# Optimization experiments

Hardware: AMD Instinct MI355X
Metric: run time of the kernel (lower is better)

## Reference

```python
import jax, jax.numpy as jnp
import numpy as np

SEQ_LEN = 4096
D_IN = 1024
D_OUT = 1024


def setup_inputs() -> dict:
    key = jax.random.key(0)
    k_x, k_q, k_k, k_v = jax.random.split(key, 4)
    s = 1.0 / np.sqrt(D_IN)
    return {
        "x": jax.random.normal(k_x, (SEQ_LEN, D_IN), dtype=jnp.float32),
        "W_query": jax.random.normal(k_q, (D_IN, D_OUT), dtype=jnp.float32) * s,
        "W_key": jax.random.normal(k_k, (D_IN, D_OUT), dtype=jnp.float32) * s,
        "W_value": jax.random.normal(k_v, (D_IN, D_OUT), dtype=jnp.float32) * s,
    }


def reference(x, W_query, W_key, W_value):
    # QKV projections (Linear without bias): [S, d_out]
    q = x @ W_query
    k = x @ W_key
    v = x @ W_value
    # Full S x S score matrix, causal mask, scaled softmax
    scores = q @ k.T  # [S, S]
    seq_len = x.shape[0]
    causal = jnp.tril(jnp.ones((seq_len, seq_len), dtype=bool))
    scores = jnp.where(causal, scores, -jnp.inf)
    scale = 1.0 / jnp.sqrt(jnp.asarray(k.shape[-1], dtype=scores.dtype))
    attn = jax.nn.softmax(scores * scale, axis=-1)
    return attn @ v  # [S, d_out]
```

## Files before the change

### kernel.cpp

```cpp
#include <hip/hip_runtime.h>
#include <math.h>

#define SEQ 4096
#define DIM 1024

typedef unsigned short u16;
typedef __attribute__((ext_vector_type(8))) short short8;
typedef __attribute__((ext_vector_type(4))) float floatx4;
typedef __attribute__((ext_vector_type(4))) unsigned short us4;

__device__ __forceinline__ float bf2f(u16 u) {
    union { unsigned int i; float f; } c; c.i = ((unsigned int)u) << 16; return c.f;
}
__device__ __forceinline__ u16 f2bf(float f) {
    union { float f; unsigned int i; } c; c.f = f;
    return (u16)((c.i + 0x7fffu + ((c.i >> 16) & 1u)) >> 16);
}
__device__ __forceinline__ void gload_lds16(const u16* g, u16* l) {
    __builtin_amdgcn_global_load_lds((const __attribute__((address_space(1))) void*)g,
                                     (__attribute__((address_space(3))) void*)l, 16, 0, 0);
}

__device__ __forceinline__ void pipe256(const u16* __restrict__ A,
                                        const u16* __restrict__ B,
                                        u16 (&As)[2][8192], u16 (&Bs)[2][4096],
                                        int lda, int ldb, int row0, int col0,
                                        int wave, int lane,
                                        floatx4 (&acc)[4][4]) {
    const int wm = wave & 3, wn = wave >> 2;
    const int sa0 = wave * 128 + lane, sa1 = sa0 + 64;
    const int ra0 = sa0 >> 2, qa0 = ((sa0 & 3) ^ ((sa0 >> 3) & 3)) * 8;
    const int ra1 = sa1 >> 2, qa1 = ((sa1 & 3) ^ ((sa1 >> 3) & 3)) * 8;
    const int sb0 = wave * 64 + lane;
    const int rb0 = sb0 >> 2, qb0 = ((sb0 & 3) ^ ((sb0 >> 3) & 3)) * 8;
    const u16* aP0 = A + (size_t)(row0 + ra0) * lda + qa0;
    const u16* aP1 = A + (size_t)(row0 + ra1) * lda + qa1;
    const u16* bP0 = B + (size_t)(col0 + rb0) * ldb + qb0;
    const int lA = wave * 1024;
    const int lB = wave * 512;
    const int frow = lane & 15;
    const int xq = (((lane >> 4) ^ ((frow >> 1) & 3))) * 8;

    auto stage = [&](int c) {
        gload_lds16(aP0, &As[c][lA]);
        gload_lds16(aP1, &As[c][lA + 512]);
        gload_lds16(bP0, &Bs[c][lB]);
        aP0 += 32; aP1 += 32; bP0 += 32;
    };

    stage(0);
    __syncthreads();
    for (int it = 0; it < 32; ++it) {
        const int cur = it & 1;
        if (it < 31) stage(cur ^ 1);
        short8 af[4], bfr[4];
#pragma unroll
        for (int t = 0; t < 4; ++t) {
            af[t]  = *(const short8*)&As[cur][(wm * 64 + t * 16 + frow) * 32 + xq];
            bfr[t] = *(const short8*)&Bs[cur][(wn * 64 + t * 16 + frow) * 32 + xq];
        }
#pragma unroll
        for (int mt = 0; mt < 4; ++mt)
#pragma unroll
            for (int nt = 0; nt < 4; ++nt)
                acc[mt][nt] = __builtin_amdgcn_mfma_f32_16x16x32_bf16(
                    af[mt], bfr[nt], acc[mt][nt], 0, 0, 0);
        __syncthreads();
    }
}

__global__ __launch_bounds__(512) void proj256(const u16* __restrict__ xb,
                                               const u16* __restrict__ Wt,
                                               u16* __restrict__ QK,
                                               u16* __restrict__ Vt,
                                               float scale0) {
    __shared__ u16 As[2][8192], Bs[2][4096];
    const int row0 = blockIdx.y * 256;
    const int col0 = blockIdx.x * 128;
    const int tid = threadIdx.x, wave = tid >> 6, lane = tid & 63;
    const int wm = wave & 3, wn = wave >> 2;

    floatx4 acc[4][4] = {};
    pipe256(xb, Wt, As, Bs, DIM, DIM, row0, col0, wave, lane, acc);

    const int cr = (lane >> 4) * 4, cc = lane & 15;
    if (col0 >= 2048) {
#pragma unroll
        for (int mt = 0; mt < 4; ++mt)
#pragma unroll
            for (int nt = 0; nt < 4; ++nt) {
                const int row = row0 + wm * 64 + mt * 16 + cr;
                const int col = (col0 - 2048) + wn * 64 + nt * 16 + cc;
                us4 o = { f2bf(acc[mt][nt][0]), f2bf(acc[mt][nt][1]),
                          f2bf(acc[mt][nt][2]), f2bf(acc[mt][nt][3]) };
                *(us4*)&Vt[(size_t)col * SEQ + row] = o;
            }
    } else {
        const float sc = (col0 < 1024) ? scale0 : 1.0f;
#pragma unroll
        for (int mt = 0; mt < 4; ++mt)
#pragma unroll
            for (int nt = 0; nt < 4; ++nt)
#pragma unroll
                for (int r = 0; r < 4; ++r) {
                    const int row = row0 + wm * 64 + mt * 16 + cr + r;
                    const int col = col0 + wn * 64 + nt * 16 + cc;
                    QK[(size_t)row * 2048 + col] = f2bf(acc[mt][nt][r] * sc);
                }
    }
}

__global__ __launch_bounds__(512) void scores256(const u16* __restrict__ QK,
                                                 u16* __restrict__ E,
                                                 float* __restrict__ Lsum) {
    __shared__ u16 As[2][8192], Bs[2][4096];
    const int t = blockIdx.x;
    int R = (int)((sqrtf(4.0f * t + 1.0f) - 1.0f) * 0.5f);
    while ((R + 1) * (R + 2) + R + 1 - 1 < t + 1) ++R;
    while (R * R + R > t) --R;
    const int bx = t - (R * R + R);
    const int row0 = R * 256, col0 = bx * 128;
    const int tid = threadIdx.x, wave = tid >> 6, lane = tid & 63;
    const int wm = wave & 3, wn = wave >> 2;

    floatx4 acc[4][4] = {};
    pipe256(QK, QK + 1024, As, Bs, 2048, 2048, row0, col0, wave, lane, acc);

    const int cr = (lane >> 4) * 4, cc = lane & 15;
#pragma unroll
    for (int mt = 0; mt < 4; ++mt) {
#pragma unroll
        for (int r = 0; r < 4; ++r) {
            const int grow = row0 + wm * 64 + mt * 16 + cr + r;
            float rowsum = 0.f;
#pragma unroll
            for (int nt = 0; nt < 4; ++nt) {
                const int gcol = col0 + wn * 64 + nt * 16 + cc;
                const float e = (gcol <= grow) ? __expf(acc[mt][nt][r]) : 0.f;
                rowsum += e;
                E[(size_t)grow * SEQ + gcol] = f2bf(e);
            }
            rowsum += __shfl_xor(rowsum, 1);
            rowsum += __shfl_xor(rowsum, 2);
            rowsum += __shfl_xor(rowsum, 4);
            rowsum += __shfl_xor(rowsum, 8);
            if (cc == 0) atomicAdd(&Lsum[grow], rowsum);
        }
    }
}

__global__ __launch_bounds__(256) void pv64(const u16* __restrict__ E,
                                            const u16* __restrict__ Vt,
                                            float* __restrict__ O,
                                            const float* __restrict__ Lsum) {
    const int lin = blockIdx.x + (blockIdx.y << 4);
    const int c = lin & 7;
    const int j = lin >> 3;
    const int x = j & 15;
    const int m = j >> 4;
    const unsigned long long PK = 0x2F3F20301F0F1000ULL;
    const int base = (int)((PK >> (m * 8)) & 0x3F);
    const int r = base + ((m & 2) ? -c : c);
    const int row0 = r * 64;
    const int col0 = x * 64;
    const int kend = row0 + 64;

    __shared__ u16 As[3][2048], Bs[3][2048];

    const int tid  = threadIdx.x;
    const int wave = tid >> 6;
    const int lane = tid & 63;
    const int wm = wave & 1;
    const int wn = wave >> 1;

    const int s0 = wave * 64 + lane;
    const int r0 = s0 >> 2, q0 = ((s0 & 3) ^ ((s0 >> 3) & 3)) * 8;
    const u16* aP = E  + (size_t)(row0 + r0) * SEQ + q0;
    const u16* bP = Vt + (size_t)(col0 + r0) * SEQ + q0;
    const int l0 = wave * 512;

    floatx4 acc[2][2] = {};
    const int niter = kend >> 5;
    const int frow = lane & 15;
    const int xq = (((lane >> 4) ^ ((frow >> 1) & 3))) * 8;
    const int mrow0 = wm * 32, nrow0 = wn * 32;

    auto stage = [&](int cb) {
        gload_lds16(aP, &As[cb][l0]);
        gload_lds16(bP, &Bs[cb][l0]);
        aP += 32; bP += 32;
    };
    stage(0);
    stage(1);

    auto compute_tile = [&](int cb) {
        short8 af[2], bfr[2];
#pragma unroll
        for (int t = 0; t < 2; ++t) {
            af[t]  = *(const short8*)&As[cb][(mrow0 + t * 16 + frow) * 32 + xq];
            bfr[t] = *(const short8*)&Bs[cb][(nrow0 + t * 16 + frow) * 32 + xq];
        }
#pragma unroll
        for (int mt = 0; mt < 2; ++mt)
#pragma unroll
            for (int nt = 0; nt < 2; ++nt)
                acc[mt][nt] = __builtin_amdgcn_mfma_f32_16x16x32_bf16(
                    af[mt], bfr[nt], acc[mt][nt], 0, 0, 0);
    };

    int cur = 0, pre = 2;
    for (int it = 0; it < niter - 2; ++it) {
        asm volatile("s_waitcnt vmcnt(2)\n\ts_barrier" ::: "memory");
        short8 af[2], bfr[2];
#pragma unroll
        for (int t = 0; t < 2; ++t) {
            af[t]  = *(const short8*)&As[cur][(mrow0 + t * 16 + frow) * 32 + xq];
            bfr[t] = *(const short8*)&Bs[cur][(nrow0 + t * 16 + frow) * 32 + xq];
        }
        stage(pre);
#pragma unroll
        for (int mt = 0; mt < 2; ++mt)
#pragma unroll
            for (int nt = 0; nt < 2; ++nt)
                acc[mt][nt] = __builtin_amdgcn_mfma_f32_16x16x32_bf16(
                    af[mt], bfr[nt], acc[mt][nt], 0, 0, 0);
        cur = (cur == 2) ? 0 : cur + 1;
        pre = (pre == 2) ? 0 : pre + 1;
    }
    asm volatile("s_waitcnt vmcnt(2)\n\ts_barrier" ::: "memory");
    compute_tile(cur);
    cur = (cur == 2) ? 0 : cur + 1;
    asm volatile("s_waitcnt vmcnt(0)\n\ts_barrier" ::: "memory");
    compute_tile(cur);

    const int cr = (lane >> 4) * 4, cc = lane & 15;
#pragma unroll
    for (int mt = 0; mt < 2; ++mt)
#pragma unroll
        for (int rr = 0; rr < 4; ++rr) {
            const int grow = row0 + wm * 32 + mt * 16 + cr + rr;
            const float invl = __builtin_amdgcn_rcpf(Lsum[grow]);
#pragma unroll
            for (int nt = 0; nt < 2; ++nt) {
                const int col = col0 + wn * 32 + nt * 16 + cc;
                O[(size_t)grow * DIM + col] = acc[mt][nt][rr] * invl;
            }
        }
}

__global__ __launch_bounds__(256) void prep(const float* __restrict__ x,
                                            const float* __restrict__ W0,
                                            const float* __restrict__ W1,
                                            const float* __restrict__ W2,
                                            u16* __restrict__ xb,
                                            u16* __restrict__ Wt,
                                            float* __restrict__ Lsum) {
    __shared__ float tile[32][33];
    const int b = blockIdx.x;
    const int tid = threadIdx.x;
    if (b < 4096) {
        const size_t i = ((size_t)b * 256 + tid) * 4;
        const float4 v = *(const float4*)(x + i);
        us4 o = { f2bf(v.x), f2bf(v.y), f2bf(v.z), f2bf(v.w) };
        *(us4*)(xb + i) = o;
    } else if (b < 7168) {
        const int t = b - 4096;
        const int z = t >> 10;
        const int idx = t & 1023;
        const float* W = (z == 0) ? W0 : (z == 1) ? W1 : W2;
        u16* out = Wt + (size_t)z * DIM * DIM;
        const int bx = (idx & 31) * 32;
        const int by = (idx >> 5) * 32;
        const int tx = tid & 31;
        const int ty = (tid >> 5) * 4;
#pragma unroll
        for (int r = 0; r < 4; ++r)
            tile[ty + r][tx] = W[(size_t)(by + ty + r) * DIM + bx + tx];
        __syncthreads();
#pragma unroll
        for (int r = 0; r < 4; ++r)
            out[(size_t)(bx + ty + r) * DIM + by + tx] = f2bf(tile[tx][ty + r]);
    } else {
        const int t = b - 7168;
        *(float4*)(Lsum + (size_t)(t * 256 + tid) * 4) =
            make_float4(0.f, 0.f, 0.f, 0.f);
    }
}

extern "C" void kernel_launch(void* const* d_in, const int* in_sizes, int n_in,
                              void* d_out, int out_size, void* d_ws, size_t ws_size,
                              hipStream_t stream) {
    const float* x  = (const float*)d_in[0];
    const float* Wq = (const float*)d_in[1];
    const float* Wk = (const float*)d_in[2];
    const float* Wv = (const float*)d_in[3];

    u16* xb    = (u16*)d_ws;
    u16* Wt    = xb  + (size_t)SEQ * DIM;
    u16* QK    = Wt  + (size_t)3072 * DIM;
    u16* Vt    = QK  + (size_t)SEQ * 2048;
    u16* E     = Vt  + (size_t)DIM * SEQ;
    float* Lsum = (float*)(E + (size_t)SEQ * SEQ);

    prep<<<7172, 256, 0, stream>>>(x, Wq, Wk, Wv, xb, Wt, Lsum);

    proj256<<<dim3(24, 16), 512, 0, stream>>>(xb, Wt, QK, Vt, 0.03125f);

    scores256<<<272, 512, 0, stream>>>(QK, E, Lsum);

    pv64<<<dim3(16, 64), 256, 0, stream>>>(E, Vt, (float*)d_out, Lsum);
}
```

Baseline: 189.3 us.

## Use 128x256 GEMM tiles with triple-buffered LDS and vmcnt-gated barriers

The shared GEMM pipeline used by the projection and score kernels changes from 256x128 tiles on 8 waves to 128x256 tiles on 4 waves. Each wave now computes an 8x4 grid of MFMA fragments, and the launch bounds allow two blocks per CU. LDS goes from double to triple buffering: loads are issued two stages ahead, and a single barrier per iteration uses explicit s_waitcnt vmcnt, replacing the trailing __syncthreads. The causal tile index mapping for scores is redone for the new tile shape. In exchange, register pressure rises from 32 accumulators per wave and LDS use per block grows.

```diff
diff --git a/kernel.cpp b/kernel.cpp
--- a/kernel.cpp
+++ b/kernel.cpp
@@ -21,76 +21,113 @@
                                      (__attribute__((address_space(3))) void*)l, 16, 0, 0);
 }
 
-__device__ __forceinline__ void pipe256(const u16* __restrict__ A,
-                                        const u16* __restrict__ B,
-                                        u16 (&As)[2][8192], u16 (&Bs)[2][4096],
-                                        int lda, int ldb, int row0, int col0,
-                                        int wave, int lane,
-                                        floatx4 (&acc)[4][4]) {
-    const int wm = wave & 3, wn = wave >> 2;
-    const int sa0 = wave * 128 + lane, sa1 = sa0 + 64;
-    const int ra0 = sa0 >> 2, qa0 = ((sa0 & 3) ^ ((sa0 >> 3) & 3)) * 8;
-    const int ra1 = sa1 >> 2, qa1 = ((sa1 & 3) ^ ((sa1 >> 3) & 3)) * 8;
-    const int sb0 = wave * 64 + lane;
-    const int rb0 = sb0 >> 2, qb0 = ((sb0 & 3) ^ ((sb0 >> 3) & 3)) * 8;
-    const u16* aP0 = A + (size_t)(row0 + ra0) * lda + qa0;
-    const u16* aP1 = A + (size_t)(row0 + ra1) * lda + qa1;
-    const u16* bP0 = B + (size_t)(col0 + rb0) * ldb + qb0;
+__device__ __forceinline__ void pipe128x256(const u16* __restrict__ A,
+                                            const u16* __restrict__ B,
+                                            u16 (&As)[3][4096], u16 (&Bs)[3][8192],
+                                            int lda, int ldb, int row0, int col0,
+                                            int wave, int lane,
+                                            floatx4 (&acc)[8][4]) {
+    const int sA0 = wave * 128 + lane;
+    const int sA1 = sA0 + 64;
+    const int rA0 = sA0 >> 2, qA0 = ((sA0 & 3) ^ ((sA0 >> 3) & 3)) * 8;
+    const int rA1 = sA1 >> 2, qA1 = ((sA1 & 3) ^ ((sA1 >> 3) & 3)) * 8;
+    const int sB0 = wave * 256 + lane;
+    const int sB1 = sB0 + 64, sB2 = sB0 + 128, sB3 = sB0 + 192;
+    const int rB0 = sB0 >> 2, qB0 = ((sB0 & 3) ^ ((sB0 >> 3) & 3)) * 8;
+    const int rB1 = sB1 >> 2, qB1 = ((sB1 & 3) ^ ((sB1 >> 3) & 3)) * 8;
+    const int rB2 = sB2 >> 2, qB2 = ((sB2 & 3) ^ ((sB2 >> 3) & 3)) * 8;
+    const int rB3 = sB3 >> 2, qB3 = ((sB3 & 3) ^ ((sB3 >> 3) & 3)) * 8;
+
+    const u16* aP0 = A + (size_t)(row0 + rA0) * lda + qA0;
+    const u16* aP1 = A + (size_t)(row0 + rA1) * lda + qA1;
+    const u16* bP0 = B + (size_t)(col0 + rB0) * ldb + qB0;
+    const u16* bP1 = B + (size_t)(col0 + rB1) * ldb + qB1;
+    const u16* bP2 = B + (size_t)(col0 + rB2) * ldb + qB2;
+    const u16* bP3 = B + (size_t)(col0 + rB3) * ldb + qB3;
     const int lA = wave * 1024;
-    const int lB = wave * 512;
+    const int lB = wave * 2048;
     const int frow = lane & 15;
     const int xq = (((lane >> 4) ^ ((frow >> 1) & 3))) * 8;
+    const int nrow0 = wave * 64;
 
     auto stage = [&](int c) {
         gload_lds16(aP0, &As[c][lA]);
         gload_lds16(aP1, &As[c][lA + 512]);
         gload_lds16(bP0, &Bs[c][lB]);
-        aP0 += 32; aP1 += 32; bP0 += 32;
+        gload_lds16(bP1, &Bs[c][lB + 512]);
+        gload_lds16(bP2, &Bs[c][lB + 1024]);
+        gload_lds16(bP3, &Bs[c][lB + 1536]);
+        aP0 += 32; aP1 += 32; bP0 += 32; bP1 += 32; bP2 += 32; bP3 += 32;
     };
 
     stage(0);
-    __syncthreads();
-    for (int it = 0; it < 32; ++it) {
-        const int cur = it & 1;
-        if (it < 31) stage(cur ^ 1);
-        short8 af[4], bfr[4];
-#pragma unroll
-        for (int t = 0; t < 4; ++t) {
-            af[t]  = *(const short8*)&As[cur][(wm * 64 + t * 16 + frow) * 32 + xq];
-            bfr[t] = *(const short8*)&Bs[cur][(wn * 64 + t * 16 + frow) * 32 + xq];
-        }
-#pragma unroll
-        for (int mt = 0; mt < 4; ++mt)
+    stage(1);
+
+    auto compute_tile = [&](int c) {
+        short8 af[8], bfr[4];
+#pragma unroll
+        for (int t = 0; t < 8; ++t)
+            af[t] = *(const short8*)&As[c][(t * 16 + frow) * 32 + xq];
+#pragma unroll
+        for (int t = 0; t < 4; ++t)
+            bfr[t] = *(const short8*)&Bs[c][(nrow0 + t * 16 + frow) * 32 + xq];
+#pragma unroll
+        for (int mt = 0; mt < 8; ++mt)
 #pragma unroll
             for (int nt = 0; nt < 4; ++nt)
                 acc[mt][nt] = __builtin_amdgcn_mfma_f32_16x16x32_bf16(
                     af[mt], bfr[nt], acc[mt][nt], 0, 0, 0);
-        __syncthreads();
-    }
-}
-
-__global__ __launch_bounds__(512) void proj256(const u16* __restrict__ xb,
+    };
+
+    int cur = 0, pre = 2;
+    for (int it = 0; it < 30; ++it) {
+        asm volatile("s_waitcnt vmcnt(6)\n\ts_barrier" ::: "memory");
+        short8 af[8], bfr[4];
+#pragma unroll
+        for (int t = 0; t < 8; ++t)
+            af[t] = *(const short8*)&As[cur][(t * 16 + frow) * 32 + xq];
+#pragma unroll
+        for (int t = 0; t < 4; ++t)
+            bfr[t] = *(const short8*)&Bs[cur][(nrow0 + t * 16 + frow) * 32 + xq];
+        stage(pre);
+#pragma unroll
+        for (int mt = 0; mt < 8; ++mt)
+#pragma unroll
+            for (int nt = 0; nt < 4; ++nt)
+                acc[mt][nt] = __builtin_amdgcn_mfma_f32_16x16x32_bf16(
+                    af[mt], bfr[nt], acc[mt][nt], 0, 0, 0);
+        cur = (cur == 2) ? 0 : cur + 1;
+        pre = (pre == 2) ? 0 : pre + 1;
+    }
+    asm volatile("s_waitcnt vmcnt(6)\n\ts_barrier" ::: "memory");
+    compute_tile(cur);
+    cur = (cur == 2) ? 0 : cur + 1;
+    asm volatile("s_waitcnt vmcnt(0)\n\ts_barrier" ::: "memory");
+    compute_tile(cur);
+}
+
+__global__ __launch_bounds__(256, 2) void proj(const u16* __restrict__ xb,
                                                const u16* __restrict__ Wt,
                                                u16* __restrict__ QK,
                                                u16* __restrict__ Vt,
                                                float scale0) {
-    __shared__ u16 As[2][8192], Bs[2][4096];
-    const int row0 = blockIdx.y * 256;
-    const int col0 = blockIdx.x * 128;
+    __shared__ u16 As[3][4096], Bs[3][8192];
+    const int row0 = blockIdx.y * 128;
+    const int col0 = blockIdx.x * 256;
     const int tid = threadIdx.x, wave = tid >> 6, lane = tid & 63;
-    const int wm = wave & 3, wn = wave >> 2;
-
-    floatx4 acc[4][4] = {};
-    pipe256(xb, Wt, As, Bs, DIM, DIM, row0, col0, wave, lane, acc);
+
+    floatx4 acc[8][4] = {};
+    pipe128x256(xb, Wt, As, Bs, DIM, DIM, row0, col0, wave, lane, acc);
 
     const int cr = (lane >> 4) * 4, cc = lane & 15;
+    const int nrow0 = wave * 64;
     if (col0 >= 2048) {
 #pragma unroll
-        for (int mt = 0; mt < 4; ++mt)
+        for (int mt = 0; mt < 8; ++mt)
 #pragma unroll
             for (int nt = 0; nt < 4; ++nt) {
-                const int row = row0 + wm * 64 + mt * 16 + cr;
-                const int col = (col0 - 2048) + wn * 64 + nt * 16 + cc;
+                const int row = row0 + mt * 16 + cr;
+                const int col = (col0 - 2048) + nrow0 + nt * 16 + cc;
                 us4 o = { f2bf(acc[mt][nt][0]), f2bf(acc[mt][nt][1]),
                           f2bf(acc[mt][nt][2]), f2bf(acc[mt][nt][3]) };
                 *(us4*)&Vt[(size_t)col * SEQ + row] = o;
@@ -98,44 +135,46 @@
     } else {
         const float sc = (col0 < 1024) ? scale0 : 1.0f;
 #pragma unroll
-        for (int mt = 0; mt < 4; ++mt)
+        for (int mt = 0; mt < 8; ++mt)
 #pragma unroll
             for (int nt = 0; nt < 4; ++nt)
 #pragma unroll
                 for (int r = 0; r < 4; ++r) {
-                    const int row = row0 + wm * 64 + mt * 16 + cr + r;
-                    const int col = col0 + wn * 64 + nt * 16 + cc;
+                    const int row = row0 + mt * 16 + cr + r;
+                    const int col = col0 + nrow0 + nt * 16 + cc;
                     QK[(size_t)row * 2048 + col] = f2bf(acc[mt][nt][r] * sc);
                 }
     }
 }
 
-__global__ __launch_bounds__(512) void scores256(const u16* __restrict__ QK,
+__global__ __launch_bounds__(256, 2) void scores(const u16* __restrict__ QK,
                                                  u16* __restrict__ E,
                                                  float* __restrict__ Lsum) {
-    __shared__ u16 As[2][8192], Bs[2][4096];
+    __shared__ u16 As[3][4096], Bs[3][8192];
     const int t = blockIdx.x;
-    int R = (int)((sqrtf(4.0f * t + 1.0f) - 1.0f) * 0.5f);
-    while ((R + 1) * (R + 2) + R + 1 - 1 < t + 1) ++R;
-    while (R * R + R > t) --R;
-    const int bx = t - (R * R + R);
-    const int row0 = R * 256, col0 = bx * 128;
+    int k = (int)sqrtf((float)t);
+    while (k > 0 && k * k + k > t) --k;
+    while ((k + 1) * (k + 1) + (k + 1) <= t) ++k;
+    int R, bx;
+    if (t < (k + 1) * (k + 1)) { R = 2 * k;     bx = t - (k * k + k); }
+    else                       { R = 2 * k + 1; bx = t - (k + 1) * (k + 1); }
+    const int row0 = R * 128, col0 = bx * 256;
     const int tid = threadIdx.x, wave = tid >> 6, lane = tid & 63;
-    const int wm = wave & 3, wn = wave >> 2;
-
-    floatx4 acc[4][4] = {};
-    pipe256(QK, QK + 1024, As, Bs, 2048, 2048, row0, col0, wave, lane, acc);
+
+    floatx4 acc[8][4] = {};
+    pipe128x256(QK, QK + 1024, As, Bs, 2048, 2048, row0, col0, wave, lane, acc);
 
     const int cr = (lane >> 4) * 4, cc = lane & 15;
-#pragma unroll
-    for (int mt = 0; mt < 4; ++mt) {
+    const int nrow0 = wave * 64;
+#pragma unroll
+    for (int mt = 0; mt < 8; ++mt) {
 #pragma unroll
         for (int r = 0; r < 4; ++r) {
-            const int grow = row0 + wm * 64 + mt * 16 + cr + r;
+            const int grow = row0 + mt * 16 + cr + r;
             float rowsum = 0.f;
 #pragma unroll
             for (int nt = 0; nt < 4; ++nt) {
-                const int gcol = col0 + wn * 64 + nt * 16 + cc;
+                const int gcol = col0 + nrow0 + nt * 16 + cc;
                 const float e = (gcol <= grow) ? __expf(acc[mt][nt][r]) : 0.f;
                 rowsum += e;
                 E[(size_t)grow * SEQ + gcol] = f2bf(e);
@@ -304,9 +343,9 @@
 
     prep<<<7172, 256, 0, stream>>>(x, Wq, Wk, Wv, xb, Wt, Lsum);
 
-    proj256<<<dim3(24, 16), 512, 0, stream>>>(xb, Wt, QK, Vt, 0.03125f);
-
-    scores256<<<272, 512, 0, stream>>>(QK, E, Lsum);
+    proj<<<dim3(12, 32), 256, 0, stream>>>(xb, Wt, QK, Vt, 0.03125f);
+
+    scores<<<272, 256, 0, stream>>>(QK, E, Lsum);
 
     pv64<<<dim3(16, 64), 256, 0, stream>>>(E, Vt, (float*)d_out, Lsum);
 }
```

Result: no change. 193.0 us (+2.0%).

## Deepen GEMM pipeline to six LDS stages and flip tiles to 128x256

Applied to the files above, without the earlier changes.

Replaces the double-buffered 256x128 GEMM mainloop with a six-buffer pipeline. It keeps four stages in flight, waits via explicit vmcnt, uses one barrier per two k-steps, and loads both steps' fragments before issuing the next loads. The projection and score kernels switch to 128-row by 256-column tiles, and the triangular block mapping for causal scores is recomputed to match. This aims to hide global-load latency and halve barrier count. In exchange, LDS use triples to about 144KB per block, which may limit occupancy.

```diff
diff --git a/kernel.cpp b/kernel.cpp
--- a/kernel.cpp
+++ b/kernel.cpp
@@ -21,67 +21,104 @@
                                      (__attribute__((address_space(3))) void*)l, 16, 0, 0);
 }
 
-__device__ __forceinline__ void pipe256(const u16* __restrict__ A,
-                                        const u16* __restrict__ B,
-                                        u16 (&As)[2][8192], u16 (&Bs)[2][4096],
-                                        int lda, int ldb, int row0, int col0,
-                                        int wave, int lane,
-                                        floatx4 (&acc)[4][4]) {
-    const int wm = wave & 3, wn = wave >> 2;
-    const int sa0 = wave * 128 + lane, sa1 = sa0 + 64;
-    const int ra0 = sa0 >> 2, qa0 = ((sa0 & 3) ^ ((sa0 >> 3) & 3)) * 8;
-    const int ra1 = sa1 >> 2, qa1 = ((sa1 & 3) ^ ((sa1 >> 3) & 3)) * 8;
-    const int sb0 = wave * 64 + lane;
-    const int rb0 = sb0 >> 2, qb0 = ((sb0 & 3) ^ ((sb0 >> 3) & 3)) * 8;
-    const u16* aP0 = A + (size_t)(row0 + ra0) * lda + qa0;
-    const u16* aP1 = A + (size_t)(row0 + ra1) * lda + qa1;
-    const u16* bP0 = B + (size_t)(col0 + rb0) * ldb + qb0;
-    const int lA = wave * 1024;
-    const int lB = wave * 512;
+__device__ __forceinline__ void pipe6(const u16* __restrict__ A,
+                                      const u16* __restrict__ B,
+                                      u16 (&As)[6][4096], u16 (&Bs)[6][8192],
+                                      int lda, int ldb, int row0, int col0,
+                                      int wave, int lane,
+                                      floatx4 (&acc)[4][4]) {
+    const int wm = wave >> 2, wn = wave & 3;
+    const int sA = wave * 64 + lane;
+    const int rA = sA >> 2, qA = ((sA & 3) ^ ((sA >> 3) & 3)) * 8;
+    const int sB0 = wave * 128 + lane, sB1 = sB0 + 64;
+    const int rB0 = sB0 >> 2, qB0 = ((sB0 & 3) ^ ((sB0 >> 3) & 3)) * 8;
+    const int rB1 = sB1 >> 2, qB1 = ((sB1 & 3) ^ ((sB1 >> 3) & 3)) * 8;
+
+    const u16* aP  = A + (size_t)(row0 + rA)  * lda + qA;
+    const u16* bP0 = B + (size_t)(col0 + rB0) * ldb + qB0;
+    const u16* bP1 = B + (size_t)(col0 + rB1) * ldb + qB1;
+    const int lA = wave * 512;
+    const int lB = wave * 1024;
     const int frow = lane & 15;
     const int xq = (((lane >> 4) ^ ((frow >> 1) & 3))) * 8;
-
-    auto stage = [&](int c) {
-        gload_lds16(aP0, &As[c][lA]);
-        gload_lds16(aP1, &As[c][lA + 512]);
-        gload_lds16(bP0, &Bs[c][lB]);
-        aP0 += 32; aP1 += 32; bP0 += 32;
+    const int mrow0 = wm * 64, nrow0 = wn * 64;
+
+    auto stage = [&](int b) {
+        gload_lds16(aP,  &As[b][lA]);
+        gload_lds16(bP0, &Bs[b][lB]);
+        gload_lds16(bP1, &Bs[b][lB + 512]);
+        aP += 32; bP0 += 32; bP1 += 32;
     };
 
-    stage(0);
-    __syncthreads();
-    for (int it = 0; it < 32; ++it) {
-        const int cur = it & 1;
-        if (it < 31) stage(cur ^ 1);
-        short8 af[4], bfr[4];
+    auto compute2 = [&](int b0, int b1) {
+#pragma unroll
+        for (int half = 0; half < 2; ++half) {
+            const int b = half ? b1 : b0;
+            short8 af[4], bfr[4];
+#pragma unroll
+            for (int t = 0; t < 4; ++t) {
+                af[t]  = *(const short8*)&As[b][(mrow0 + t * 16 + frow) * 32 + xq];
+                bfr[t] = *(const short8*)&Bs[b][(nrow0 + t * 16 + frow) * 32 + xq];
+            }
+#pragma unroll
+            for (int mt = 0; mt < 4; ++mt)
+#pragma unroll
+                for (int nt = 0; nt < 4; ++nt)
+                    acc[mt][nt] = __builtin_amdgcn_mfma_f32_16x16x32_bf16(
+                        af[mt], bfr[nt], acc[mt][nt], 0, 0, 0);
+        }
+    };
+
+    stage(0); stage(1); stage(2); stage(3);
+
+    int b = 0;
+    for (int w = 0; w < 14; ++w) {
+        asm volatile("s_waitcnt vmcnt(6)\n\ts_barrier" ::: "memory");
+        short8 af0[4], bf0[4], af1[4], bf1[4];
+        const int b1 = (b + 1) % 6;
 #pragma unroll
         for (int t = 0; t < 4; ++t) {
-            af[t]  = *(const short8*)&As[cur][(wm * 64 + t * 16 + frow) * 32 + xq];
-            bfr[t] = *(const short8*)&Bs[cur][(wn * 64 + t * 16 + frow) * 32 + xq];
-        }
+            af0[t] = *(const short8*)&As[b ][(mrow0 + t * 16 + frow) * 32 + xq];
+            bf0[t] = *(const short8*)&Bs[b ][(nrow0 + t * 16 + frow) * 32 + xq];
+            af1[t] = *(const short8*)&As[b1][(mrow0 + t * 16 + frow) * 32 + xq];
+            bf1[t] = *(const short8*)&Bs[b1][(nrow0 + t * 16 + frow) * 32 + xq];
+        }
+        stage((b + 4) % 6);
+        stage((b + 5) % 6);
 #pragma unroll
         for (int mt = 0; mt < 4; ++mt)
 #pragma unroll
             for (int nt = 0; nt < 4; ++nt)
                 acc[mt][nt] = __builtin_amdgcn_mfma_f32_16x16x32_bf16(
-                    af[mt], bfr[nt], acc[mt][nt], 0, 0, 0);
-        __syncthreads();
-    }
-}
-
-__global__ __launch_bounds__(512) void proj256(const u16* __restrict__ xb,
-                                               const u16* __restrict__ Wt,
-                                               u16* __restrict__ QK,
-                                               u16* __restrict__ Vt,
-                                               float scale0) {
-    __shared__ u16 As[2][8192], Bs[2][4096];
-    const int row0 = blockIdx.y * 256;
-    const int col0 = blockIdx.x * 128;
+                    af0[mt], bf0[nt], acc[mt][nt], 0, 0, 0);
+#pragma unroll
+        for (int mt = 0; mt < 4; ++mt)
+#pragma unroll
+            for (int nt = 0; nt < 4; ++nt)
+                acc[mt][nt] = __builtin_amdgcn_mfma_f32_16x16x32_bf16(
+                    af1[mt], bf1[nt], acc[mt][nt], 0, 0, 0);
+        b = (b + 2) % 6;
+    }
+    asm volatile("s_waitcnt vmcnt(6)\n\ts_barrier" ::: "memory");
+    compute2(b, (b + 1) % 6);
+    b = (b + 2) % 6;
+    asm volatile("s_waitcnt vmcnt(0)\n\ts_barrier" ::: "memory");
+    compute2(b, (b + 1) % 6);
+}
+
+__global__ __launch_bounds__(512) void proj(const u16* __restrict__ xb,
+                                            const u16* __restrict__ Wt,
+                                            u16* __restrict__ QK,
+                                            u16* __restrict__ Vt,
+                                            float scale0) {
+    __shared__ u16 As[6][4096], Bs[6][8192];
+    const int row0 = blockIdx.y * 128;
+    const int col0 = blockIdx.x * 256;
     const int tid = threadIdx.x, wave = tid >> 6, lane = tid & 63;
-    const int wm = wave & 3, wn = wave >> 2;
+    const int wm = wave >> 2, wn = wave & 3;
 
     floatx4 acc[4][4] = {};
-    pipe256(xb, Wt, As, Bs, DIM, DIM, row0, col0, wave, lane, acc);
+    pipe6(xb, Wt, As, Bs, DIM, DIM, row0, col0, wave, lane, acc);
 
     const int cr = (lane >> 4) * 4, cc = lane & 15;
     if (col0 >= 2048) {
@@ -110,21 +147,23 @@
     }
 }
 
-__global__ __launch_bounds__(512) void scores256(const u16* __restrict__ QK,
-                                                 u16* __restrict__ E,
-                                                 float* __restrict__ Lsum) {
-    __shared__ u16 As[2][8192], Bs[2][4096];
+__global__ __launch_bounds__(512) void scores(const u16* __restrict__ QK,
+                                              u16* __restrict__ E,
+                                              float* __restrict__ Lsum) {
+    __shared__ u16 As[6][4096], Bs[6][8192];
     const int t = blockIdx.x;
-    int R = (int)((sqrtf(4.0f * t + 1.0f) - 1.0f) * 0.5f);
-    while ((R + 1) * (R + 2) + R + 1 - 1 < t + 1) ++R;
-    while (R * R + R > t) --R;
-    const int bx = t - (R * R + R);
-    const int row0 = R * 256, col0 = bx * 128;
+    int k = (int)sqrtf((float)t);
+    while (k > 0 && k * k + k > t) --k;
+    while ((k + 1) * (k + 1) + (k + 1) <= t) ++k;
+    int R, bx;
+    if (t < (k + 1) * (k + 1)) { R = 2 * k;     bx = t - (k * k + k); }
+    else                       { R = 2 * k + 1; bx = t - (k + 1) * (k + 1); }
+    const int row0 = R * 128, col0 = bx * 256;
     const int tid = threadIdx.x, wave = tid >> 6, lane = tid & 63;
-    const int wm = wave & 3, wn = wave >> 2;
+    const int wm = wave >> 2, wn = wave & 3;
 
     floatx4 acc[4][4] = {};
-    pipe256(QK, QK + 1024, As, Bs, 2048, 2048, row0, col0, wave, lane, acc);
+    pipe6(QK, QK + 1024, As, Bs, 2048, 2048, row0, col0, wave, lane, acc);
 
     const int cr = (lane >> 4) * 4, cc = lane & 15;
 #pragma unroll
@@ -304,9 +343,9 @@
 
     prep<<<7172, 256, 0, stream>>>(x, Wq, Wk, Wv, xb, Wt, Lsum);
 
-    proj256<<<dim3(24, 16), 512, 0, stream>>>(xb, Wt, QK, Vt, 0.03125f);
-
-    scores256<<<272, 512, 0, stream>>>(QK, E, Lsum);
+    proj<<<dim3(12, 32), 512, 0, stream>>>(xb, Wt, QK, Vt, 0.03125f);
+
+    scores<<<272, 512, 0, stream>>>(QK, E, Lsum);
 
     pv64<<<dim3(16, 64), 256, 0, stream>>>(E, Vt, (float*)d_out, Lsum);
 }
```

After: 192.1 us. No clear change (+1.5%).

## Use 256x256 tiles with 4-stage LDS pipeline and phased MFMA scheduling

Applied to the files above, without the earlier changes.

Replaces the 256x128 double-buffered GEMM mainloop used by the projection and score kernels with a 256x256 tile and a four-slot LDS ring. Global-to-LDS loads are interleaved with MFMA phases, waited on with explicit vmcnt-based barriers, and the MFMA sections run at raised wave priority. The aim is better data reuse per tile and overlap of memory latency with compute. In exchange, grid sizes are halved (192 and 136 blocks), which may underfill the CUs, and register and LDS pressure rise.

```diff
diff --git a/kernel.cpp b/kernel.cpp
--- a/kernel.cpp
+++ b/kernel.cpp
@@ -21,75 +21,114 @@
                                      (__attribute__((address_space(3))) void*)l, 16, 0, 0);
 }
 
-__device__ __forceinline__ void pipe256(const u16* __restrict__ A,
+template <int VM> __device__ __forceinline__ void vmbar() {
+    if constexpr (VM == 8)
+        asm volatile("s_waitcnt vmcnt(8)\n\ts_barrier" ::: "memory");
+    else if constexpr (VM == 4)
+        asm volatile("s_waitcnt vmcnt(4)\n\ts_barrier" ::: "memory");
+    else
+        asm volatile("s_waitcnt vmcnt(0)\n\ts_barrier" ::: "memory");
+}
+
+__device__ __forceinline__ void pipe8ph(const u16* __restrict__ A,
                                         const u16* __restrict__ B,
-                                        u16 (&As)[2][8192], u16 (&Bs)[2][4096],
+                                        u16 (&As)[4][8192], u16 (&Bs)[4][8192],
                                         int lda, int ldb, int row0, int col0,
                                         int wave, int lane,
-                                        floatx4 (&acc)[4][4]) {
-    const int wm = wave & 3, wn = wave >> 2;
-    const int sa0 = wave * 128 + lane, sa1 = sa0 + 64;
-    const int ra0 = sa0 >> 2, qa0 = ((sa0 & 3) ^ ((sa0 >> 3) & 3)) * 8;
-    const int ra1 = sa1 >> 2, qa1 = ((sa1 & 3) ^ ((sa1 >> 3) & 3)) * 8;
-    const int sb0 = wave * 64 + lane;
-    const int rb0 = sb0 >> 2, qb0 = ((sb0 & 3) ^ ((sb0 >> 3) & 3)) * 8;
-    const u16* aP0 = A + (size_t)(row0 + ra0) * lda + qa0;
-    const u16* aP1 = A + (size_t)(row0 + ra1) * lda + qa1;
-    const u16* bP0 = B + (size_t)(col0 + rb0) * ldb + qb0;
-    const int lA = wave * 1024;
-    const int lB = wave * 512;
+                                        floatx4 (&acc)[8][4]) {
+    const int wm = wave >> 2, wn = wave & 3;
+    const int s0 = wave * 128 + lane, s1 = s0 + 64;
+    const int rA0 = s0 >> 2, qA0 = ((s0 & 3) ^ ((s0 >> 3) & 3)) * 8;
+    const int rA1 = s1 >> 2, qA1 = ((s1 & 3) ^ ((s1 >> 3) & 3)) * 8;
+    const u16* aP0 = A + (size_t)(row0 + rA0) * lda + qA0;
+    const u16* aP1 = A + (size_t)(row0 + rA1) * lda + qA1;
+    const u16* bP0 = B + (size_t)(col0 + rA0) * ldb + qA0;
+    const u16* bP1 = B + (size_t)(col0 + rA1) * ldb + qA1;
+    const int l0 = wave * 1024;
     const int frow = lane & 15;
     const int xq = (((lane >> 4) ^ ((frow >> 1) & 3))) * 8;
-
-    auto stage = [&](int c) {
-        gload_lds16(aP0, &As[c][lA]);
-        gload_lds16(aP1, &As[c][lA + 512]);
-        gload_lds16(bP0, &Bs[c][lB]);
-        aP0 += 32; aP1 += 32; bP0 += 32;
-    };
-
-    stage(0);
-    __syncthreads();
-    for (int it = 0; it < 32; ++it) {
-        const int cur = it & 1;
-        if (it < 31) stage(cur ^ 1);
-        short8 af[4], bfr[4];
-#pragma unroll
-        for (int t = 0; t < 4; ++t) {
-            af[t]  = *(const short8*)&As[cur][(wm * 64 + t * 16 + frow) * 32 + xq];
-            bfr[t] = *(const short8*)&Bs[cur][(wn * 64 + t * 16 + frow) * 32 + xq];
-        }
-#pragma unroll
-        for (int mt = 0; mt < 4; ++mt)
-#pragma unroll
-            for (int nt = 0; nt < 4; ++nt)
-                acc[mt][nt] = __builtin_amdgcn_mfma_f32_16x16x32_bf16(
-                    af[mt], bfr[nt], acc[mt][nt], 0, 0, 0);
-        __syncthreads();
-    }
-}
-
-__global__ __launch_bounds__(512) void proj256(const u16* __restrict__ xb,
-                                               const u16* __restrict__ Wt,
-                                               u16* __restrict__ QK,
-                                               u16* __restrict__ Vt,
-                                               float scale0) {
-    __shared__ u16 As[2][8192], Bs[2][4096];
+    const int arow = wm * 128, bcol = wn * 64;
+
+    auto stageFull = [&](int slot) {
+        gload_lds16(aP0, &As[slot][l0]);
+        gload_lds16(aP1, &As[slot][l0 + 512]);
+        gload_lds16(bP0, &Bs[slot][l0]);
+        gload_lds16(bP1, &Bs[slot][l0 + 512]);
+        aP0 += 32; aP1 += 32; bP0 += 32; bP1 += 32;
+    };
+    auto stage1 = [&](int slot, int kind) {
+        if (kind == 0)      { gload_lds16(aP0, &As[slot][l0]);       aP0 += 32; }
+        else if (kind == 1) { gload_lds16(aP1, &As[slot][l0 + 512]); aP1 += 32; }
+        else if (kind == 2) { gload_lds16(bP0, &Bs[slot][l0]);       bP0 += 32; }
+        else                { gload_lds16(bP1, &Bs[slot][l0 + 512]); bP1 += 32; }
+    };
+
+    auto half = [&](int b, int sslot, bool doStage) {
+#pragma unroll
+        for (int mq = 0; mq < 2; ++mq) {
+            short8 af[4];
+#pragma unroll
+            for (int t = 0; t < 4; ++t)
+                af[t] = *(const short8*)
+                    &As[b][(arow + mq * 64 + t * 16 + frow) * 32 + xq];
+#pragma unroll
+            for (int nq = 0; nq < 2; ++nq) {
+                short8 bf[2];
+#pragma unroll
+                for (int v = 0; v < 2; ++v)
+                    bf[v] = *(const short8*)
+                        &Bs[b][(bcol + nq * 32 + v * 16 + frow) * 32 + xq];
+                if (doStage) stage1(sslot, mq * 2 + nq);
+                asm volatile("s_barrier" ::: "memory");
+                asm volatile("s_waitcnt lgkmcnt(0)" ::: "memory");
+                __builtin_amdgcn_sched_barrier(0);
+                __builtin_amdgcn_s_setprio(1);
+#pragma unroll
+                for (int t = 0; t < 4; ++t)
+#pragma unroll
+                    for (int v = 0; v < 2; ++v)
+                        acc[mq * 4 + t][nq * 2 + v] =
+                            __builtin_amdgcn_mfma_f32_16x16x32_bf16(
+                                af[t], bf[v], acc[mq * 4 + t][nq * 2 + v],
+                                0, 0, 0);
+                __builtin_amdgcn_s_setprio(0);
+                asm volatile("s_barrier" ::: "memory");
+            }
+        }
+    };
+
+    stageFull(0); stageFull(1); stageFull(2);
+
+    for (int h = 0; h < 29; ++h) {
+        vmbar<8>();
+        half(h & 3, (h + 3) & 3, true);
+    }
+    vmbar<8>(); half(1, 0, false);
+    vmbar<4>(); half(2, 0, false);
+    vmbar<0>(); half(3, 0, false);
+}
+
+__global__ __launch_bounds__(512) void proj(const u16* __restrict__ xb,
+                                            const u16* __restrict__ Wt,
+                                            u16* __restrict__ QK,
+                                            u16* __restrict__ Vt,
+                                            float scale0) {
+    __shared__ u16 As[4][8192], Bs[4][8192];
     const int row0 = blockIdx.y * 256;
-    const int col0 = blockIdx.x * 128;
+    const int col0 = blockIdx.x * 256;
     const int tid = threadIdx.x, wave = tid >> 6, lane = tid & 63;
-    const int wm = wave & 3, wn = wave >> 2;
-
-    floatx4 acc[4][4] = {};
-    pipe256(xb, Wt, As, Bs, DIM, DIM, row0, col0, wave, lane, acc);
+    const int wm = wave >> 2, wn = wave & 3;
+
+    floatx4 acc[8][4] = {};
+    pipe8ph(xb, Wt, As, Bs, DIM, DIM, row0, col0, wave, lane, acc);
 
     const int cr = (lane >> 4) * 4, cc = lane & 15;
     if (col0 >= 2048) {
 #pragma unroll
-        for (int mt = 0; mt < 4; ++mt)
+        for (int mt = 0; mt < 8; ++mt)
 #pragma unroll
             for (int nt = 0; nt < 4; ++nt) {
-                const int row = row0 + wm * 64 + mt * 16 + cr;
+                const int row = row0 + wm * 128 + mt * 16 + cr;
                 const int col = (col0 - 2048) + wn * 64 + nt * 16 + cc;
                 us4 o = { f2bf(acc[mt][nt][0]), f2bf(acc[mt][nt][1]),
                           f2bf(acc[mt][nt][2]), f2bf(acc[mt][nt][3]) };
@@ -98,40 +137,40 @@
     } else {
         const float sc = (col0 < 1024) ? scale0 : 1.0f;
 #pragma unroll
-        for (int mt = 0; mt < 4; ++mt)
+        for (int mt = 0; mt < 8; ++mt)
 #pragma unroll
             for (int nt = 0; nt < 4; ++nt)
 #pragma unroll
                 for (int r = 0; r < 4; ++r) {
-                    const int row = row0 + wm * 64 + mt * 16 + cr + r;
+                    const int row = row0 + wm * 128 + mt * 16 + cr + r;
                     const int col = col0 + wn * 64 + nt * 16 + cc;
                     QK[(size_t)row * 2048 + col] = f2bf(acc[mt][nt][r] * sc);
                 }
     }
 }
 
-__global__ __launch_bounds__(512) void scores256(const u16* __restrict__ QK,
-                                                 u16* __restrict__ E,
-                                                 float* __restrict__ Lsum) {
-    __shared__ u16 As[2][8192], Bs[2][4096];
+__global__ __launch_bounds__(512) void scores(const u16* __restrict__ QK,
+                                              u16* __restrict__ E,
+                                              float* __restrict__ Lsum) {
+    __shared__ u16 As[4][8192], Bs[4][8192];
     const int t = blockIdx.x;
-    int R = (int)((sqrtf(4.0f * t + 1.0f) - 1.0f) * 0.5f);
-    while ((R + 1) * (R + 2) + R + 1 - 1 < t + 1) ++R;
-    while (R * R + R > t) --R;
-    const int bx = t - (R * R + R);
-    const int row0 = R * 256, col0 = bx * 128;
+    int by = (int)((sqrtf(8.0f * t + 1.0f) - 1.0f) * 0.5f);
+    while ((by + 1) * (by + 2) / 2 <= t) ++by;
+    while (by * (by + 1) / 2 > t) --by;
+    const int bx = t - by * (by + 1) / 2;
+    const int row0 = by * 256, col0 = bx * 256;
     const int tid = threadIdx.x, wave = tid >> 6, lane = tid & 63;
-    const int wm = wave & 3, wn = wave >> 2;
-
-    floatx4 acc[4][4] = {};
-    pipe256(QK, QK + 1024, As, Bs, 2048, 2048, row0, col0, wave, lane, acc);
+    const int wm = wave >> 2, wn = wave & 3;
+
+    floatx4 acc[8][4] = {};
+    pipe8ph(QK, QK + 1024, As, Bs, 2048, 2048, row0, col0, wave, lane, acc);
 
     const int cr = (lane >> 4) * 4, cc = lane & 15;
 #pragma unroll
-    for (int mt = 0; mt < 4; ++mt) {
+    for (int mt = 0; mt < 8; ++mt) {
 #pragma unroll
         for (int r = 0; r < 4; ++r) {
-            const int grow = row0 + wm * 64 + mt * 16 + cr + r;
+            const int grow = row0 + wm * 128 + mt * 16 + cr + r;
             float rowsum = 0.f;
 #pragma unroll
             for (int nt = 0; nt < 4; ++nt) {
@@ -304,9 +343,9 @@
 
     prep<<<7172, 256, 0, stream>>>(x, Wq, Wk, Wv, xb, Wt, Lsum);
 
-    proj256<<<dim3(24, 16), 512, 0, stream>>>(xb, Wt, QK, Vt, 0.03125f);
-
-    scores256<<<272, 512, 0, stream>>>(QK, E, Lsum);
+    proj<<<dim3(12, 16), 512, 0, stream>>>(xb, Wt, QK, Vt, 0.03125f);
+
+    scores<<<136, 512, 0, stream>>>(QK, E, Lsum);
 
     pv64<<<dim3(16, 64), 256, 0, stream>>>(E, Vt, (float*)d_out, Lsum);
 }
```

Result: slower. 213.6 us (+12.8%).
